# Kernel tuning notes

Measured on AMD Instinct MI355X. Metric: run time of the kernel, lower is better.

## Reference

```python
import jax, jax.numpy as jnp
import numpy as np

PS = 8            # patch_size
GRID = 8          # img_size // patch_size
N_PATCHES = 64
PATCH_DIM = 192   # 3 * 8 * 8
CENTRAL = np.array([r * 8 + c for r in range(2, 6) for c in range(2, 6)], dtype=np.int32)  # 16 patches
AGENT = np.array([r * 8 + c for r in range(3, 6) for c in range(3, 6)], dtype=np.int32)    # 9 patches
EPS = 1e-8


def setup_inputs() -> dict:
    key = jax.random.key(0)
    k1, k2, k3, k4, k5 = jax.random.split(key, 5)
    B, K, E, V = 1024, 4096, 2048, 2048
    pixels = jax.random.uniform(k1, (B, 3, 64, 64), dtype=jnp.float32)
    codebook = jax.random.normal(k2, (K, PATCH_DIM), dtype=jnp.float32)
    codebook = codebook / jnp.clip(jnp.linalg.norm(codebook, axis=1, keepdims=True), EPS)
    embeddings = jax.random.normal(k3, (K, E), dtype=jnp.float32)
    codebook_vsa = jax.random.randint(k4, (K, V), 0, 2).astype(jnp.float32)
    position_roles = jax.random.randint(k5, (N_PATCHES, V), 0, 2).astype(jnp.float32)
    return {"pixels": pixels, "codebook": codebook, "embeddings": embeddings,
            "codebook_vsa": codebook_vsa, "position_roles": position_roles}


def _patchify(pixels):
    # (B,3,64,64) -> (B,64,192), matching torch unfold/permute order (gh, gw, C, ph, pw)
    B = pixels.shape[0]
    x = pixels.reshape(B, 3, GRID, PS, GRID, PS)          # (B,C,gh,ph,gw,pw)
    x = jnp.transpose(x, (0, 2, 4, 1, 3, 5))              # (B,gh,gw,C,ph,pw)
    return x.reshape(B, N_PATCHES, PATCH_DIM)


def reference(pixels, codebook, embeddings, codebook_vsa, position_roles):
    patches = _patchify(pixels)                                            # (B,64,192)
    patches_norm = patches / jnp.clip(
        jnp.linalg.norm(patches, axis=2, keepdims=True), EPS)
    sim = jnp.einsum('bpd,kd->bpk', patches_norm, codebook)                # (B,64,4096)
    indices = jnp.argmax(sim, axis=2)                                      # (B,64) int
    embeds = embeddings[indices]                                           # (B,64,2048)
    z_real = embeds.mean(axis=1)                                           # (B,2048)
    z_local = embeds[:, AGENT, :].mean(axis=1)                             # (B,2048)
    # VSA bind + bundle over the 16 central patches
    idx_c = indices[:, CENTRAL]                                            # (B,16)
    cb_vecs = codebook_vsa[idx_c]                                          # (B,16,V)
    pos = position_roles[CENTRAL]                                          # (16,V)
    bound = jnp.mod(cb_vecs + pos[None, :, :], 2.0)                        # XOR on {0,1}
    summed = bound.sum(axis=1)                                             # (B,V)
    z_vsa = (summed > (len(CENTRAL) / 2)).astype(jnp.float32)
    return z_real, z_vsa, indices, z_local
```

## Files before the change

kernel.cpp:

```cpp
#include <hip/hip_runtime.h>
#include <hip/hip_bf16.h>
#include <math.h>

#define NIMG 1024
#define NPATCH 64
#define PDIM 192
#define KCODES 4096
#define EDIM 2048
#define VDIM 2048
#define MROWS (NIMG * NPATCH)
#define KP 192
#define NKS 6
#define NCT 16

typedef _Float16 f16x8 __attribute__((ext_vector_type(8)));
typedef __attribute__((ext_vector_type(4))) float f32x4;

__device__ __forceinline__ void gload_lds16(const void* g, void* l) {
    __builtin_amdgcn_global_load_lds(
        (const __attribute__((address_space(1))) unsigned int*)g,
        (__attribute__((address_space(3))) unsigned int*)l,
        16, 0, 0);
}

__device__ __forceinline__ void merge_top2(float& v1, int& i1, float& v2, int& i2,
                                           float ov1, int oi1, float ov2, int oi2) {
    bool aw = (v1 > ov1) || (v1 == ov1 && i1 < oi1);
    float w1v = aw ? v1 : ov1;  int w1i = aw ? i1 : oi1;
    float c2v = aw ? v2 : ov2;  int c2i = aw ? i2 : oi2;
    float l1v = aw ? ov1 : v1;  int l1i = aw ? oi1 : i1;
    bool bw = (c2v > l1v) || (c2v == l1v && c2i < l1i);
    v1 = w1v; i1 = w1i;
    v2 = bw ? c2v : l1v; i2 = bw ? c2i : l1i;
}

__device__ __forceinline__ void kfold(int& t1, int& t2, int key) {
    int m = (key < t1) ? key : t1;
    t2 = (t2 > m) ? t2 : m;
    t1 = (t1 > key) ? t1 : key;
}

__global__ __launch_bounds__(256) void prep_codebook_kernel(
    const float* __restrict__ cb, unsigned short* __restrict__ Bh)
{
    int i = (blockIdx.x * 256 + threadIdx.x) * 8;
    if (i >= KCODES * PDIM) return;
    float4 u = *(const float4*)(cb + i);
    float4 v = *(const float4*)(cb + i + 4);
    f16x8 h;
    h[0] = (_Float16)u.x; h[1] = (_Float16)u.y; h[2] = (_Float16)u.z; h[3] = (_Float16)u.w;
    h[4] = (_Float16)v.x; h[5] = (_Float16)v.y; h[6] = (_Float16)v.z; h[7] = (_Float16)v.w;
    *(f16x8*)(Bh + i) = h;
}

__global__ __launch_bounds__(512, 2) void gemm_top2_kernel(
    const float* __restrict__ pixels, const unsigned short* __restrict__ B,
    float* __restrict__ o1v, int* __restrict__ o1i,
    float* __restrict__ o2v, int* __restrict__ o2i)
{
    __shared__ unsigned short Asl[6][8192];
    __shared__ unsigned short Bsl[3][8192];

    const int t = threadIdx.x;
    const int w = t >> 6;
    const int l = t & 63;
    const int lo4 = l & 15, hi4 = l >> 4;
    const int wr = w >> 1, wc = w & 1;
    const int m0 = blockIdx.x * 256;

    const float* pixb = pixels + (size_t)(m0 >> 6) * 12288;
    if (t < 256) {
        int p = t & 63;
        const float* pp = pixb + (size_t)(t >> 6) * 12288 + (p >> 3) * 512 + (p & 7) * 8;
        float s = 0.f;
        #pragma unroll
        for (int c3 = 0; c3 < 3; ++c3)
            #pragma unroll
            for (int rr = 0; rr < 8; ++rr) {
                const float* q = pp + c3 * 4096 + rr * 64;
                float4 u = *(const float4*)q, v = *(const float4*)(q + 4);
                s += u.x*u.x + u.y*u.y + u.z*u.z + u.w*u.w
                   + v.x*v.x + v.y*v.y + v.z*v.z + v.w*v.w;
            }
        ((float*)Asl)[t] = 1.f / fmaxf(sqrtf(s), 1e-8f);
    }
    __syncthreads();
    const int prow = t & 255;
    const float rinv = ((float*)Asl)[prow];
    __syncthreads();
    {
        int p = prow & 63;
        const float* pp = pixb + (size_t)(prow >> 6) * 12288 + (p >> 3) * 512 + (p & 7) * 8;
        const int ch0 = (t >> 8) * 12;
        #pragma unroll
        for (int q = 0; q < 12; ++q) {
            int ch = ch0 + q;
            const float* src = pp + (ch >> 3) * 4096 + (ch & 7) * 64;
            float4 u = *(const float4*)src, v = *(const float4*)(src + 4);
            f16x8 hv;
            hv[0] = (_Float16)(u.x * rinv); hv[1] = (_Float16)(u.y * rinv);
            hv[2] = (_Float16)(u.z * rinv); hv[3] = (_Float16)(u.w * rinv);
            hv[4] = (_Float16)(v.x * rinv); hv[5] = (_Float16)(v.y * rinv);
            hv[6] = (_Float16)(v.z * rinv); hv[7] = (_Float16)(v.w * rinv);
            int j = ch >> 2, c = ch & 3;
            *(f16x8*)&Asl[j][prow * 32 + ((c ^ ((prow >> 1) & 3)) * 8)] = hv;
        }
    }

    const int srow = t >> 2;
    const int kc   = (t & 3) ^ ((srow >> 1) & 3);
    const unsigned short* b0b = B + (size_t)srow * KP + kc * 8;

    int aoff[4], boff[8];
    #pragma unroll
    for (int rt = 0; rt < 4; ++rt) {
        int row = wr * 64 + rt * 16 + lo4;
        aoff[rt] = row * 32 + (hi4 ^ ((row >> 1) & 3)) * 8;
    }
    #pragma unroll
    for (int cf = 0; cf < 8; ++cf) {
        int col = wc * 128 + cf * 16 + lo4;
        boff[cf] = col * 32 + (hi4 ^ ((col >> 1) & 3)) * 8;
    }

    int t1k[16], t2k[16];
    #pragma unroll
    for (int e = 0; e < 16; ++e) { t1k[e] = (int)0x80000000; t2k[e] = (int)0x80000000; }

    auto stageB = [&](int sct, int sj, int sbuf) {
        char* Bd = (char*)Bsl[sbuf] + w * 1024;
        const unsigned short* gb = b0b + sct * (256 * KP) + sj * 32;
        gload_lds16(gb, Bd);
        gload_lds16(gb + 128 * KP, Bd + 8192);
    };

    stageB(0, 0, 0);
    stageB(0, 1, 1);
    asm volatile("s_waitcnt vmcnt(2) lgkmcnt(0)\n\ts_barrier" ::: "memory");

    f32x4 acc[4][8];
    f16x8 af[4];
    #pragma unroll
    for (int rt = 0; rt < 4; ++rt) af[rt] = *(const f16x8*)&Asl[0][aoff[rt]];

    int bb = 0, sb = 2;
    int stct = 0, stj = 2;

    for (int ct = 0; ct < NCT; ++ct) {
      for (int j = 0; j < NKS; ++j) {
        const unsigned short* Bb = Bsl[bb];
        const int jn = (j + 1) % NKS;

        f16x8 bg[4];
        #pragma unroll
        for (int cf = 0; cf < 4; ++cf) bg[cf] = *(const f16x8*)&Bb[boff[cf]];
        if (stct < NCT) stageB(stct, stj, sb);

        if (j == 0) {
            #pragma unroll
            for (int i = 0; i < 4; ++i)
                #pragma unroll
                for (int jj = 0; jj < 8; ++jj) acc[i][jj] = (f32x4){0.f, 0.f, 0.f, 0.f};
        }

        asm volatile("s_waitcnt lgkmcnt(0)" ::: "memory");
        __builtin_amdgcn_sched_barrier(0);
        __builtin_amdgcn_s_setprio(1);
        #pragma unroll
        for (int rt = 0; rt < 4; ++rt)
            #pragma unroll
            for (int cf = 0; cf < 4; ++cf)
                acc[rt][cf] = __builtin_amdgcn_mfma_f32_16x16x32_f16(af[rt], bg[cf], acc[rt][cf], 0, 0, 0);
        __builtin_amdgcn_s_setprio(0);

        f16x8 bh[4];
        #pragma unroll
        for (int cf = 0; cf < 4; ++cf) bh[cf] = *(const f16x8*)&Bb[boff[cf + 4]];

        asm volatile("s_waitcnt lgkmcnt(0)" ::: "memory");
        __builtin_amdgcn_sched_barrier(0);
        __builtin_amdgcn_s_setprio(1);
        #pragma unroll
        for (int rt = 0; rt < 4; ++rt)
            #pragma unroll
            for (int cf = 0; cf < 4; ++cf)
                acc[rt][cf + 4] = __builtin_amdgcn_mfma_f32_16x16x32_f16(af[rt], bh[cf], acc[rt][cf + 4], 0, 0, 0);
        __builtin_amdgcn_s_setprio(0);
        __builtin_amdgcn_sched_barrier(0);

        #pragma unroll
        for (int rt = 0; rt < 4; ++rt) af[rt] = *(const f16x8*)&Asl[jn][aoff[rt]];

        if (j == NKS - 1) {
            #pragma unroll
            for (int cf = 0; cf < 8; ++cf) {
                const int inv7 = 0x7F ^ ((ct << 3) | cf);
                #pragma unroll
                for (int rt = 0; rt < 4; ++rt)
                    #pragma unroll
                    for (int r = 0; r < 4; ++r) {
                        int key = (__float_as_int(acc[rt][cf][r]) & ~0x7F) | inv7;
                        kfold(t1k[rt * 4 + r], t2k[rt * 4 + r], key);
                    }
            }
        }

        if (ct < NCT - 1 || j < NKS - 2) {
            asm volatile("s_waitcnt vmcnt(2)\n\ts_barrier" ::: "memory");
        } else if (j == NKS - 2) {
            asm volatile("s_waitcnt vmcnt(0)\n\ts_barrier" ::: "memory");
        }

        if (stct < NCT && ++stj == NKS) { stj = 0; ++stct; }
        if (++bb == 3) bb = 0;
        if (++sb == 3) sb = 0;
      }
    }

    float p1v[16], p2v[16];
    int   p1i[16], p2i[16];
    #pragma unroll
    for (int e = 0; e < 16; ++e) {
        p1v[e] = __int_as_float(t1k[e] & ~0x7F);
        int lo7 = 0x7F ^ (t1k[e] & 0x7F);
        p1i[e] = ((lo7 >> 3) << 8) + wc * 128 + ((lo7 & 7) << 4) + lo4;
        p2v[e] = __int_as_float(t2k[e] & ~0x7F);
        int lo7b = 0x7F ^ (t2k[e] & 0x7F);
        p2i[e] = ((lo7b >> 3) << 8) + wc * 128 + ((lo7b & 7) << 4) + lo4;
    }

    #pragma unroll
    for (int e = 0; e < 16; ++e) {
        #pragma unroll
        for (int m = 1; m < 16; m <<= 1) {
            float ov1 = __shfl_xor(p1v[e], m);
            int   oi1 = __shfl_xor(p1i[e], m);
            float ov2 = __shfl_xor(p2v[e], m);
            int   oi2 = __shfl_xor(p2i[e], m);
            merge_top2(p1v[e], p1i[e], p2v[e], p2i[e], ov1, oi1, ov2, oi2);
        }
    }

    __syncthreads();
    float* r1v = (float*)Asl;
    float* r2v = r1v + 512;
    int*   r1i = (int*)(r2v + 512);
    int*   r2i = r1i + 512;
    if (lo4 == 0) {
        #pragma unroll
        for (int rt = 0; rt < 4; ++rt)
            #pragma unroll
            for (int r = 0; r < 4; ++r) {
                const int e = rt * 4 + r;
                int row = wr * 64 + rt * 16 + hi4 * 4 + r;
                r1v[row * 2 + wc] = p1v[e]; r1i[row * 2 + wc] = p1i[e];
                r2v[row * 2 + wc] = p2v[e]; r2i[row * 2 + wc] = p2i[e];
            }
    }
    __syncthreads();
    if (t < 256) {
        float v1 = r1v[t * 2], v2 = r2v[t * 2];
        int   i1 = r1i[t * 2], i2 = r2i[t * 2];
        merge_top2(v1, i1, v2, i2, r1v[t * 2 + 1], r1i[t * 2 + 1],
                                   r2v[t * 2 + 1], r2i[t * 2 + 1]);
        int grow = m0 + t;
        o1v[grow] = v1; o1i[grow] = i1;
        o2v[grow] = v2; o2i[grow] = i2;
    }
}

__global__ __launch_bounds__(256) void refine_kernel(
    const float* __restrict__ pixels, const float* __restrict__ codebook,
    const float* __restrict__ o1v, const int* __restrict__ o1i,
    const float* __restrict__ o2v, const int* __restrict__ o2i,
    int* __restrict__ idx_out, float* __restrict__ idxf_out)
{
    int row = blockIdx.x * 256 + threadIdx.x;
    if (row >= MROWS) return;
    float v1 = o1v[row], v2 = o2v[row];
    int   i1 = o1i[row], i2 = o2i[row];
    int idx = i1;
    if (v1 - v2 <= 4e-4f) {
        int b = row >> 6, p = row & 63;
        int gr = p >> 3, gc = p & 7;
        const float* pb = pixels + (size_t)b * 3 * 4096 + gr * 8 * 64 + gc * 8;
        const float* c1 = codebook + (size_t)i1 * PDIM;
        const float* c2 = codebook + (size_t)i2 * PDIM;
        double s1 = 0.0, s2 = 0.0;
        for (int d = 0; d < PDIM; ++d) {
            int ch = d >> 6, r = (d >> 3) & 7, c = d & 7;
            double x = (double)pb[ch * 4096 + r * 64 + c];
            s1 += x * (double)c1[d];
            s2 += x * (double)c2[d];
        }
        if (s2 > s1 || (s2 == s1 && i2 < i1)) idx = i2;
    }
    idx_out[row] = idx;
    idxf_out[row] = (float)idx;
}

__global__ __launch_bounds__(256) void zv_kernel(
    const float* __restrict__ emb, const float* __restrict__ vsa,
    const float* __restrict__ roles, const int* __restrict__ idx,
    float* __restrict__ z_real, float* __restrict__ z_local,
    float* __restrict__ z_vsa)
{
    __shared__ int sidx[64];
    int b = blockIdx.x, t = threadIdx.x;
    if (t < 64) sidx[t] = idx[b * 64 + t];
    __syncthreads();
    float s[8], sl[8];
    #pragma unroll
    for (int j = 0; j < 8; ++j) { s[j] = 0.f; sl[j] = 0.f; }
    for (int p = 0; p < 64; ++p) {
        int gr = p >> 3, gc = p & 7;
        bool ag = (gr >= 3 && gr < 6 && gc >= 3 && gc < 6);
        const float* er = emb + (size_t)sidx[p] * EDIM + t * 8;
        float v[8];
        *(float4*)&v[0] = *(const float4*)er;
        *(float4*)&v[4] = *(const float4*)(er + 4);
        #pragma unroll
        for (int j = 0; j < 8; ++j) s[j] += v[j];
        if (ag) {
            #pragma unroll
            for (int j = 0; j < 8; ++j) sl[j] += v[j];
        }
    }
    float* zr = z_real + (size_t)b * EDIM + t * 8;
    float* zl = z_local + (size_t)b * EDIM + t * 8;
    #pragma unroll
    for (int j = 0; j < 8; ++j) {
        zr[j] = s[j] * (1.f / 64.f);
        zl[j] = sl[j] * (1.f / 9.f);
    }

    float cnt[8];
    #pragma unroll
    for (int j = 0; j < 8; ++j) cnt[j] = 0.f;
    for (int cp = 0; cp < 16; ++cp) {
        int p = (2 + (cp >> 2)) * 8 + 2 + (cp & 3);
        const float* vr = vsa + (size_t)sidx[p] * VDIM + t * 8;
        const float* pr = roles + (size_t)p * VDIM + t * 8;
        float a[8], r[8];
        *(float4*)&a[0] = *(const float4*)vr;
        *(float4*)&a[4] = *(const float4*)(vr + 4);
        *(float4*)&r[0] = *(const float4*)pr;
        *(float4*)&r[4] = *(const float4*)(pr + 4);
        #pragma unroll
        for (int j = 0; j < 8; ++j) cnt[j] += (a[j] != r[j]) ? 1.f : 0.f;
    }
    #pragma unroll
    for (int j = 0; j < 8; ++j)
        z_vsa[(size_t)b * VDIM + t * 8 + j] = cnt[j] > 8.f ? 1.f : 0.f;
}

extern "C" void kernel_launch(void* const* d_in, const int* in_sizes, int n_in,
                              void* d_out, int out_size, void* d_ws, size_t ws_size,
                              hipStream_t stream) {
    const float* pixels         = (const float*)d_in[0];
    const float* codebook       = (const float*)d_in[1];
    const float* embeddings     = (const float*)d_in[2];
    const float* codebook_vsa   = (const float*)d_in[3];
    const float* position_roles = (const float*)d_in[4];

    float* out     = (float*)d_out;
    float* z_real  = out;
    float* z_vsa   = out + 2097152;
    float* idxf    = out + 4194304;
    float* z_local = out + 4259840;

    char* ws = (char*)d_ws;
    unsigned short* Bh = (unsigned short*)(ws);
    float* o1v = (float*)(ws + 1572864);
    int*   o1i = (int*)  (ws + 1835008);
    float* o2v = (float*)(ws + 2097152);
    int*   o2i = (int*)  (ws + 2359296);
    int*   idxws = (int*)(ws + 2621440);

    prep_codebook_kernel<<<KCODES * PDIM / 8 / 256, 256, 0, stream>>>(codebook, Bh);

    gemm_top2_kernel<<<MROWS / 256, 512, 0, stream>>>(pixels, Bh, o1v, o1i, o2v, o2i);

    refine_kernel<<<MROWS / 256, 256, 0, stream>>>(pixels, codebook,
        o1v, o1i, o2v, o2i, idxws, idxf);
    zv_kernel<<<NIMG, 256, 0, stream>>>(embeddings, codebook_vsa, position_roles,
        idxws, z_real, z_local, z_vsa);
}
```

Measured before the change: 192.0 us.

## Double-buffer 64-wide K slabs for B and fuse patch-norm computation into one pass

The B pipeline moves from a triple buffer of 32-wide K slices to a double buffer of 64-wide slices, so each barrier covers twice as many MFMAs and the K-loop has three steps per tile instead of six. The first B prefetch is now issued before the patch normalisation, so it overlaps that prologue. The norm is computed as two half-sums by all 512 threads and combined through LDS, instead of 256 threads each reading the whole patch. In exchange, the wait is now a full vmcnt(0) with only one stage of lookahead, so global-load latency may show up at each barrier, and LDS use for B grows.

```diff
diff --git a/kernel.cpp b/kernel.cpp
--- a/kernel.cpp
+++ b/kernel.cpp
@@ -10,7 +10,7 @@
 #define VDIM 2048
 #define MROWS (NIMG * NPATCH)
 #define KP 192
-#define NKS 6
+#define NKS 3
 #define NCT 16
 
 typedef _Float16 f16x8 __attribute__((ext_vector_type(8)));
@@ -59,7 +59,7 @@
     float* __restrict__ o2v, int* __restrict__ o2i)
 {
     __shared__ unsigned short Asl[6][8192];
-    __shared__ unsigned short Bsl[3][8192];
+    __shared__ unsigned short Bsl[2][16384];
 
     const int t = threadIdx.x;
     const int w = t >> 6;
@@ -68,33 +68,46 @@
     const int wr = w >> 1, wc = w & 1;
     const int m0 = blockIdx.x * 256;
 
+    const int srow = t >> 2;
+    const int kc   = (t & 3) ^ ((srow >> 1) & 3);
+    const unsigned short* b0b = B + (size_t)srow * KP + kc * 8;
+
+    auto stageB = [&](int sct, int sj, int sbuf) {
+        char* Bd = (char*)Bsl[sbuf] + w * 1024;
+        const unsigned short* gb = b0b + sct * (256 * KP) + sj * 64;
+        gload_lds16(gb, Bd);
+        gload_lds16(gb + 128 * KP, Bd + 8192);
+        gload_lds16(gb + 32, Bd + 16384);
+        gload_lds16(gb + 32 + 128 * KP, Bd + 16384 + 8192);
+    };
+
+    stageB(0, 0, 0);
+
     const float* pixb = pixels + (size_t)(m0 >> 6) * 12288;
-    if (t < 256) {
-        int p = t & 63;
-        const float* pp = pixb + (size_t)(t >> 6) * 12288 + (p >> 3) * 512 + (p & 7) * 8;
-        float s = 0.f;
-        #pragma unroll
-        for (int c3 = 0; c3 < 3; ++c3)
-            #pragma unroll
-            for (int rr = 0; rr < 8; ++rr) {
-                const float* q = pp + c3 * 4096 + rr * 64;
-                float4 u = *(const float4*)q, v = *(const float4*)(q + 4);
-                s += u.x*u.x + u.y*u.y + u.z*u.z + u.w*u.w
-                   + v.x*v.x + v.y*v.y + v.z*v.z + v.w*v.w;
-            }
-        ((float*)Asl)[t] = 1.f / fmaxf(sqrtf(s), 1e-8f);
-    }
-    __syncthreads();
     const int prow = t & 255;
-    const float rinv = ((float*)Asl)[prow];
-    __syncthreads();
     {
         int p = prow & 63;
         const float* pp = pixb + (size_t)(prow >> 6) * 12288 + (p >> 3) * 512 + (p & 7) * 8;
-        const int ch0 = (t >> 8) * 12;
+        const int m0c = (t >> 8) * 12;
+        float s = 0.f;
         #pragma unroll
         for (int q = 0; q < 12; ++q) {
-            int ch = ch0 + q;
+            int m = m0c + q;
+            const float* src = pp + (m >> 3) * 4096 + (m & 7) * 64;
+            float4 u = *(const float4*)src, v = *(const float4*)(src + 4);
+            s += u.x*u.x + u.y*u.y + u.z*u.z + u.w*u.w
+               + v.x*v.x + v.y*v.y + v.z*v.z + v.w*v.w;
+        }
+        ((float*)Asl)[t] = s;
+        asm volatile("s_waitcnt lgkmcnt(0)" ::: "memory");
+        __builtin_amdgcn_s_barrier();
+        float tot = ((float*)Asl)[prow] + ((float*)Asl)[256 + prow];
+        float rinv = 1.f / fmaxf(sqrtf(tot), 1e-8f);
+        asm volatile("s_waitcnt lgkmcnt(0)" ::: "memory");
+        __builtin_amdgcn_s_barrier();
+        #pragma unroll
+        for (int q = 0; q < 12; ++q) {
+            int ch = m0c + q;
             const float* src = pp + (ch >> 3) * 4096 + (ch & 7) * 64;
             float4 u = *(const float4*)src, v = *(const float4*)(src + 4);
             f16x8 hv;
@@ -107,10 +120,6 @@
         }
     }
 
-    const int srow = t >> 2;
-    const int kc   = (t & 3) ^ ((srow >> 1) & 3);
-    const unsigned short* b0b = B + (size_t)srow * KP + kc * 8;
-
     int aoff[4], boff[8];
     #pragma unroll
     for (int rt = 0; rt < 4; ++rt) {
@@ -127,34 +136,23 @@
     #pragma unroll
     for (int e = 0; e < 16; ++e) { t1k[e] = (int)0x80000000; t2k[e] = (int)0x80000000; }
 
-    auto stageB = [&](int sct, int sj, int sbuf) {
-        char* Bd = (char*)Bsl[sbuf] + w * 1024;
-        const unsigned short* gb = b0b + sct * (256 * KP) + sj * 32;
-        gload_lds16(gb, Bd);
-        gload_lds16(gb + 128 * KP, Bd + 8192);
-    };
-
-    stageB(0, 0, 0);
-    stageB(0, 1, 1);
-    asm volatile("s_waitcnt vmcnt(2) lgkmcnt(0)\n\ts_barrier" ::: "memory");
+    asm volatile("s_waitcnt vmcnt(0) lgkmcnt(0)\n\ts_barrier" ::: "memory");
 
     f32x4 acc[4][8];
-    f16x8 af[4];
-    #pragma unroll
-    for (int rt = 0; rt < 4; ++rt) af[rt] = *(const f16x8*)&Asl[0][aoff[rt]];
-
-    int bb = 0, sb = 2;
-    int stct = 0, stj = 2;
+    int bb = 0;
+    int stct = 0, stj = 1;
 
     for (int ct = 0; ct < NCT; ++ct) {
       for (int j = 0; j < NKS; ++j) {
+        if (stct < NCT) stageB(stct, stj, bb ^ 1);
+
         const unsigned short* Bb = Bsl[bb];
-        const int jn = (j + 1) % NKS;
-
-        f16x8 bg[4];
+        f16x8 af[4], bg[4], bh[4];
+
+        #pragma unroll
+        for (int rt = 0; rt < 4; ++rt) af[rt] = *(const f16x8*)&Asl[2*j][aoff[rt]];
         #pragma unroll
         for (int cf = 0; cf < 4; ++cf) bg[cf] = *(const f16x8*)&Bb[boff[cf]];
-        if (stct < NCT) stageB(stct, stj, sb);
 
         if (j == 0) {
             #pragma unroll
@@ -173,10 +171,34 @@
                 acc[rt][cf] = __builtin_amdgcn_mfma_f32_16x16x32_f16(af[rt], bg[cf], acc[rt][cf], 0, 0, 0);
         __builtin_amdgcn_s_setprio(0);
 
-        f16x8 bh[4];
         #pragma unroll
         for (int cf = 0; cf < 4; ++cf) bh[cf] = *(const f16x8*)&Bb[boff[cf + 4]];
-
+        asm volatile("s_waitcnt lgkmcnt(0)" ::: "memory");
+        __builtin_amdgcn_sched_barrier(0);
+        __builtin_amdgcn_s_setprio(1);
+        #pragma unroll
+        for (int rt = 0; rt < 4; ++rt)
+            #pragma unroll
+            for (int cf = 0; cf < 4; ++cf)
+                acc[rt][cf + 4] = __builtin_amdgcn_mfma_f32_16x16x32_f16(af[rt], bh[cf], acc[rt][cf + 4], 0, 0, 0);
+        __builtin_amdgcn_s_setprio(0);
+
+        #pragma unroll
+        for (int rt = 0; rt < 4; ++rt) af[rt] = *(const f16x8*)&Asl[2*j+1][aoff[rt]];
+        #pragma unroll
+        for (int cf = 0; cf < 4; ++cf) bg[cf] = *(const f16x8*)&Bb[8192 + boff[cf]];
+        asm volatile("s_waitcnt lgkmcnt(0)" ::: "memory");
+        __builtin_amdgcn_sched_barrier(0);
+        __builtin_amdgcn_s_setprio(1);
+        #pragma unroll
+        for (int rt = 0; rt < 4; ++rt)
+            #pragma unroll
+            for (int cf = 0; cf < 4; ++cf)
+                acc[rt][cf] = __builtin_amdgcn_mfma_f32_16x16x32_f16(af[rt], bg[cf], acc[rt][cf], 0, 0, 0);
+        __builtin_amdgcn_s_setprio(0);
+
+        #pragma unroll
+        for (int cf = 0; cf < 4; ++cf) bh[cf] = *(const f16x8*)&Bb[8192 + boff[cf + 4]];
         asm volatile("s_waitcnt lgkmcnt(0)" ::: "memory");
         __builtin_amdgcn_sched_barrier(0);
         __builtin_amdgcn_s_setprio(1);
@@ -188,8 +210,8 @@
         __builtin_amdgcn_s_setprio(0);
         __builtin_amdgcn_sched_barrier(0);
 
-        #pragma unroll
-        for (int rt = 0; rt < 4; ++rt) af[rt] = *(const f16x8*)&Asl[jn][aoff[rt]];
+        if (ct < NCT - 1 || j < NKS - 1)
+            asm volatile("s_waitcnt vmcnt(0)\n\ts_barrier" ::: "memory");
 
         if (j == NKS - 1) {
             #pragma unroll
@@ -205,15 +227,8 @@
             }
         }
 
-        if (ct < NCT - 1 || j < NKS - 2) {
-            asm volatile("s_waitcnt vmcnt(2)\n\ts_barrier" ::: "memory");
-        } else if (j == NKS - 2) {
-            asm volatile("s_waitcnt vmcnt(0)\n\ts_barrier" ::: "memory");
-        }
-
         if (stct < NCT && ++stj == NKS) { stj = 0; ++stct; }
-        if (++bb == 3) bb = 0;
-        if (++sb == 3) sb = 0;
+        bb ^= 1;
       }
     }
 
```

Result: slower. 200.7 us (+4.5%).

## Halve GEMM block tile to 128x128 with 256 threads and split norm computation

Applied to the files above, without the earlier changes.

The fused similarity GEMM plus top-2 kernel now uses 128-row by 128-column tiles with 4 waves instead of 256x256 with 8 waves. Each wave holds a 64x64 accumulator tile, and the code-tile loop runs 32 times. Doubling the grid and cutting LDS use and register pressure per block should raise occupancy and load balance across CUs, at the cost of reloading each B tile for twice as many row blocks. The patch-norm reduction is now split across both thread halves and fused with the A staging loads, and the first B prefetches are issued before that work to overlap it.

```diff
diff --git a/kernel.cpp b/kernel.cpp
--- a/kernel.cpp
+++ b/kernel.cpp
@@ -11,7 +11,7 @@
 #define MROWS (NIMG * NPATCH)
 #define KP 192
 #define NKS 6
-#define NCT 16
+#define NCT 32
 
 typedef _Float16 f16x8 __attribute__((ext_vector_type(8)));
 typedef __attribute__((ext_vector_type(4))) float f32x4;
@@ -53,48 +53,60 @@
     *(f16x8*)(Bh + i) = h;
 }
 
-__global__ __launch_bounds__(512, 2) void gemm_top2_kernel(
+__global__ __launch_bounds__(256, 2) void gemm_top2_kernel(
     const float* __restrict__ pixels, const unsigned short* __restrict__ B,
     float* __restrict__ o1v, int* __restrict__ o1i,
     float* __restrict__ o2v, int* __restrict__ o2i)
 {
-    __shared__ unsigned short Asl[6][8192];
-    __shared__ unsigned short Bsl[3][8192];
+    __shared__ unsigned short Asl[6][4096];
+    __shared__ unsigned short Bsl[3][4096];
 
     const int t = threadIdx.x;
     const int w = t >> 6;
     const int l = t & 63;
     const int lo4 = l & 15, hi4 = l >> 4;
     const int wr = w >> 1, wc = w & 1;
-    const int m0 = blockIdx.x * 256;
+    const int m0 = blockIdx.x * 128;
+
+    const int srow = t >> 2;
+    const int kc   = (t & 3) ^ ((srow >> 1) & 3);
+    const unsigned short* b0b = B + (size_t)srow * KP + kc * 8;
+
+    auto stageB = [&](int sct, int sj, int sbuf) {
+        char* Bd = (char*)Bsl[sbuf] + w * 1024;
+        const unsigned short* gb = b0b + sct * (128 * KP) + sj * 32;
+        gload_lds16(gb, Bd);
+        gload_lds16(gb + 64 * KP, Bd + 4096);
+    };
+
+    stageB(0, 0, 0);
+    stageB(0, 1, 1);
 
     const float* pixb = pixels + (size_t)(m0 >> 6) * 12288;
-    if (t < 256) {
-        int p = t & 63;
-        const float* pp = pixb + (size_t)(t >> 6) * 12288 + (p >> 3) * 512 + (p & 7) * 8;
-        float s = 0.f;
-        #pragma unroll
-        for (int c3 = 0; c3 < 3; ++c3)
-            #pragma unroll
-            for (int rr = 0; rr < 8; ++rr) {
-                const float* q = pp + c3 * 4096 + rr * 64;
-                float4 u = *(const float4*)q, v = *(const float4*)(q + 4);
-                s += u.x*u.x + u.y*u.y + u.z*u.z + u.w*u.w
-                   + v.x*v.x + v.y*v.y + v.z*v.z + v.w*v.w;
-            }
-        ((float*)Asl)[t] = 1.f / fmaxf(sqrtf(s), 1e-8f);
-    }
-    __syncthreads();
-    const int prow = t & 255;
-    const float rinv = ((float*)Asl)[prow];
-    __syncthreads();
+    const int prow = t & 127;
     {
         int p = prow & 63;
         const float* pp = pixb + (size_t)(prow >> 6) * 12288 + (p >> 3) * 512 + (p & 7) * 8;
-        const int ch0 = (t >> 8) * 12;
+        const int m0c = (t >> 7) * 12;
+        float s = 0.f;
         #pragma unroll
         for (int q = 0; q < 12; ++q) {
-            int ch = ch0 + q;
+            int m = m0c + q;
+            const float* src = pp + (m >> 3) * 4096 + (m & 7) * 64;
+            float4 u = *(const float4*)src, v = *(const float4*)(src + 4);
+            s += u.x*u.x + u.y*u.y + u.z*u.z + u.w*u.w
+               + v.x*v.x + v.y*v.y + v.z*v.z + v.w*v.w;
+        }
+        ((float*)Asl)[t] = s;
+        asm volatile("s_waitcnt lgkmcnt(0)" ::: "memory");
+        __builtin_amdgcn_s_barrier();
+        float tot = ((float*)Asl)[prow] + ((float*)Asl)[128 + prow];
+        float rinv = 1.f / fmaxf(sqrtf(tot), 1e-8f);
+        asm volatile("s_waitcnt lgkmcnt(0)" ::: "memory");
+        __builtin_amdgcn_s_barrier();
+        #pragma unroll
+        for (int q = 0; q < 12; ++q) {
+            int ch = m0c + q;
             const float* src = pp + (ch >> 3) * 4096 + (ch & 7) * 64;
             float4 u = *(const float4*)src, v = *(const float4*)(src + 4);
             f16x8 hv;
@@ -107,19 +119,15 @@
         }
     }
 
-    const int srow = t >> 2;
-    const int kc   = (t & 3) ^ ((srow >> 1) & 3);
-    const unsigned short* b0b = B + (size_t)srow * KP + kc * 8;
-
-    int aoff[4], boff[8];
+    int aoff[4], boff[4];
     #pragma unroll
     for (int rt = 0; rt < 4; ++rt) {
         int row = wr * 64 + rt * 16 + lo4;
         aoff[rt] = row * 32 + (hi4 ^ ((row >> 1) & 3)) * 8;
     }
     #pragma unroll
-    for (int cf = 0; cf < 8; ++cf) {
-        int col = wc * 128 + cf * 16 + lo4;
+    for (int cf = 0; cf < 4; ++cf) {
+        int col = wc * 64 + cf * 16 + lo4;
         boff[cf] = col * 32 + (hi4 ^ ((col >> 1) & 3)) * 8;
     }
 
@@ -127,18 +135,9 @@
     #pragma unroll
     for (int e = 0; e < 16; ++e) { t1k[e] = (int)0x80000000; t2k[e] = (int)0x80000000; }
 
-    auto stageB = [&](int sct, int sj, int sbuf) {
-        char* Bd = (char*)Bsl[sbuf] + w * 1024;
-        const unsigned short* gb = b0b + sct * (256 * KP) + sj * 32;
-        gload_lds16(gb, Bd);
-        gload_lds16(gb + 128 * KP, Bd + 8192);
-    };
-
-    stageB(0, 0, 0);
-    stageB(0, 1, 1);
     asm volatile("s_waitcnt vmcnt(2) lgkmcnt(0)\n\ts_barrier" ::: "memory");
 
-    f32x4 acc[4][8];
+    f32x4 acc[4][4];
     f16x8 af[4];
     #pragma unroll
     for (int rt = 0; rt < 4; ++rt) af[rt] = *(const f16x8*)&Asl[0][aoff[rt]];
@@ -151,16 +150,16 @@
         const unsigned short* Bb = Bsl[bb];
         const int jn = (j + 1) % NKS;
 
-        f16x8 bg[4];
-        #pragma unroll
-        for (int cf = 0; cf < 4; ++cf) bg[cf] = *(const f16x8*)&Bb[boff[cf]];
+        f16x8 bg[2];
+        bg[0] = *(const f16x8*)&Bb[boff[0]];
+        bg[1] = *(const f16x8*)&Bb[boff[1]];
         if (stct < NCT) stageB(stct, stj, sb);
 
         if (j == 0) {
             #pragma unroll
             for (int i = 0; i < 4; ++i)
                 #pragma unroll
-                for (int jj = 0; jj < 8; ++jj) acc[i][jj] = (f32x4){0.f, 0.f, 0.f, 0.f};
+                for (int jj = 0; jj < 4; ++jj) acc[i][jj] = (f32x4){0.f, 0.f, 0.f, 0.f};
         }
 
         asm volatile("s_waitcnt lgkmcnt(0)" ::: "memory");
@@ -169,13 +168,13 @@
         #pragma unroll
         for (int rt = 0; rt < 4; ++rt)
             #pragma unroll
-            for (int cf = 0; cf < 4; ++cf)
+            for (int cf = 0; cf < 2; ++cf)
                 acc[rt][cf] = __builtin_amdgcn_mfma_f32_16x16x32_f16(af[rt], bg[cf], acc[rt][cf], 0, 0, 0);
         __builtin_amdgcn_s_setprio(0);
 
-        f16x8 bh[4];
-        #pragma unroll
-        for (int cf = 0; cf < 4; ++cf) bh[cf] = *(const f16x8*)&Bb[boff[cf + 4]];
+        f16x8 bh[2];
+        bh[0] = *(const f16x8*)&Bb[boff[2]];
+        bh[1] = *(const f16x8*)&Bb[boff[3]];
 
         asm volatile("s_waitcnt lgkmcnt(0)" ::: "memory");
         __builtin_amdgcn_sched_barrier(0);
@@ -183,8 +182,8 @@
         #pragma unroll
         for (int rt = 0; rt < 4; ++rt)
             #pragma unroll
-            for (int cf = 0; cf < 4; ++cf)
-                acc[rt][cf + 4] = __builtin_amdgcn_mfma_f32_16x16x32_f16(af[rt], bh[cf], acc[rt][cf + 4], 0, 0, 0);
+            for (int cf = 0; cf < 2; ++cf)
+                acc[rt][cf + 2] = __builtin_amdgcn_mfma_f32_16x16x32_f16(af[rt], bh[cf], acc[rt][cf + 2], 0, 0, 0);
         __builtin_amdgcn_s_setprio(0);
         __builtin_amdgcn_sched_barrier(0);
 
@@ -193,8 +192,8 @@
 
         if (j == NKS - 1) {
             #pragma unroll
-            for (int cf = 0; cf < 8; ++cf) {
-                const int inv7 = 0x7F ^ ((ct << 3) | cf);
+            for (int cf = 0; cf < 4; ++cf) {
+                const int inv7 = 0x7F ^ ((ct << 2) | cf);
                 #pragma unroll
                 for (int rt = 0; rt < 4; ++rt)
                     #pragma unroll
@@ -222,11 +221,11 @@
     #pragma unroll
     for (int e = 0; e < 16; ++e) {
         p1v[e] = __int_as_float(t1k[e] & ~0x7F);
-        int lo7 = 0x7F ^ (t1k[e] & 0x7F);
-        p1i[e] = ((lo7 >> 3) << 8) + wc * 128 + ((lo7 & 7) << 4) + lo4;
+        int e7 = 0x7F ^ (t1k[e] & 0x7F);
+        p1i[e] = ((e7 >> 2) << 7) + wc * 64 + ((e7 & 3) << 4) + lo4;
         p2v[e] = __int_as_float(t2k[e] & ~0x7F);
-        int lo7b = 0x7F ^ (t2k[e] & 0x7F);
-        p2i[e] = ((lo7b >> 3) << 8) + wc * 128 + ((lo7b & 7) << 4) + lo4;
+        int e7b = 0x7F ^ (t2k[e] & 0x7F);
+        p2i[e] = ((e7b >> 2) << 7) + wc * 64 + ((e7b & 3) << 4) + lo4;
     }
 
     #pragma unroll
@@ -243,9 +242,9 @@
 
     __syncthreads();
     float* r1v = (float*)Asl;
-    float* r2v = r1v + 512;
-    int*   r1i = (int*)(r2v + 512);
-    int*   r2i = r1i + 512;
+    float* r2v = r1v + 256;
+    int*   r1i = (int*)(r2v + 256);
+    int*   r2i = r1i + 256;
     if (lo4 == 0) {
         #pragma unroll
         for (int rt = 0; rt < 4; ++rt)
@@ -258,7 +257,7 @@
             }
     }
     __syncthreads();
-    if (t < 256) {
+    if (t < 128) {
         float v1 = r1v[t * 2], v2 = r2v[t * 2];
         int   i1 = r1i[t * 2], i2 = r2i[t * 2];
         merge_top2(v1, i1, v2, i2, r1v[t * 2 + 1], r1i[t * 2 + 1],
@@ -379,7 +378,7 @@
 
     prep_codebook_kernel<<<KCODES * PDIM / 8 / 256, 256, 0, stream>>>(codebook, Bh);
 
-    gemm_top2_kernel<<<MROWS / 256, 512, 0, stream>>>(pixels, Bh, o1v, o1i, o2v, o2i);
+    gemm_top2_kernel<<<MROWS / 128, 256, 0, stream>>>(pixels, Bh, o1v, o1i, o2v, o2i);
 
     refine_kernel<<<MROWS / 256, 256, 0, stream>>>(pixels, codebook,
         o1v, o1i, o2v, o2i, idxws, idxf);
```

After: 202.8 us. 5.6% more time.
